# Kernel optimization log

Hardware: AMD Instinct MI355X
Metric: run time of the kernel (lower is better)

## Reference

```python
import jax, jax.numpy as jnp
import numpy as np

DIM = 1024
HEADS = 16
DIM_HEAD = 64
INNER = HEADS * DIM_HEAD
SCALE = DIM_HEAD ** -0.5


def rotate_half(t):
    # '... (j d) -> ... j d' with j=2: split last dim in half
    x1, x2 = jnp.split(t, 2, axis=-1)
    return jnp.concatenate((-x2, x1), axis=-1)


def rotary_pos(n, d, dtype):
    inv_freq = 1.0 / (10000.0 ** (jnp.arange(0, d, 2, dtype=jnp.float32) / d))
    freqs = jnp.arange(n, dtype=jnp.float32)[:, None] * inv_freq[None, :]  # (n, d/2)
    return jnp.concatenate((freqs, freqs), axis=-1).astype(dtype)  # (n, d)


def apply_rope(pos, t):
    return t * jnp.cos(pos) + rotate_half(t) * jnp.sin(pos)


def setup_inputs() -> dict:
    key = jax.random.key(0)
    ks = jax.random.split(key, 5)
    x = jax.random.normal(ks[0], (2, 2048, DIM), dtype=jnp.float32)
    gamma = jnp.ones((DIM,), dtype=jnp.float32)
    beta = jnp.zeros((DIM,), dtype=jnp.float32)
    Wq = jax.random.normal(ks[1], (DIM, INNER), dtype=jnp.float32) * 0.02
    Wkv = jax.random.normal(ks[2], (DIM, 2 * INNER), dtype=jnp.float32) * 0.02
    Wo = jax.random.normal(ks[3], (INNER, DIM), dtype=jnp.float32) * 0.02
    return {"x": x, "gamma": gamma, "beta": beta, "Wq": Wq, "Wkv": Wkv, "Wo": Wo}


def reference(x, gamma, beta, Wq, Wkv, Wo):
    b, n, _ = x.shape
    # LayerNorm with learned gamma, fixed-zero beta buffer
    mu = jnp.mean(x, axis=-1, keepdims=True)
    var = jnp.var(x, axis=-1, keepdims=True)
    xn = (x - mu) / jnp.sqrt(var + 1e-5) * gamma + beta

    q = xn @ Wq                       # (b, n, inner)
    kv = xn @ Wkv
    k, v = jnp.split(kv, 2, axis=-1)

    def to_heads(t):
        return t.reshape(b, n, HEADS, DIM_HEAD).transpose(0, 2, 1, 3)  # b h n d

    q, k, v = map(to_heads, (q, k, v))

    pos = rotary_pos(n, DIM_HEAD, x.dtype)  # (n, d)
    q = apply_rope(pos, q)
    k = apply_rope(pos, k)

    q = q * SCALE
    sim = jnp.einsum('bhid,bhjd->bhij', q, k)

    neg = -jnp.finfo(sim.dtype).max
    causal_mask = jnp.triu(jnp.ones((n, n), dtype=bool), k=1)
    sim = jnp.where(causal_mask, neg, sim)

    attn = jax.nn.softmax(sim, axis=-1)
    out = jnp.einsum('bhij,bhjd->bhid', attn, v)
    out = out.transpose(0, 2, 1, 3).reshape(b, n, INNER)
    return out @ Wo
```

## Files before the change

kernel.cpp:

```cpp
#include <hip/hip_runtime.h>
#include <stdint.h>

typedef unsigned short u16;
typedef __attribute__((ext_vector_type(8))) short short8;
typedef __attribute__((ext_vector_type(4))) float floatx4;
typedef __attribute__((ext_vector_type(4))) unsigned short u16x4;
typedef __attribute__((ext_vector_type(2))) unsigned int uint2v;

__device__ __forceinline__ float bf2f(u16 v) {
  union { uint32_t u; float f; } x; x.u = ((uint32_t)v) << 16; return x.f;
}
__device__ __forceinline__ u16 f2bf(float f) {
  union { float f; uint32_t u; } x; x.f = f;
  uint32_t r = x.u + 0x7fffu + ((x.u >> 16) & 1u);
  return (u16)(r >> 16);
}
__device__ __forceinline__ uint32_t fu(float f) {
  union { float f; uint32_t u; } x; x.f = f; return x.u;
}

#define GL2LDS(g, l)                                                          \
  __builtin_amdgcn_global_load_lds(                                           \
      (const __attribute__((address_space(1))) void*)(g),                     \
      (__attribute__((address_space(3))) void*)(l), 16, 0, 0)

#define WAITBAR(N)                                                            \
  asm volatile("s_waitcnt vmcnt(" #N ")\n\ts_barrier" ::: "memory")
#define BARX asm volatile("s_barrier" ::: "memory")
#define VM0BARX asm volatile("s_waitcnt vmcnt(0)\n\ts_barrier" ::: "memory")

__global__ __launch_bounds__(256) void prep_k(const float* __restrict__ x,
                                              const float* __restrict__ gamma,
                                              const float* __restrict__ beta,
                                              const float* __restrict__ Wq,
                                              const float* __restrict__ Wkv,
                                              const float* __restrict__ Wo,
                                              u16* __restrict__ xn,
                                              u16* __restrict__ wqkvT,
                                              u16* __restrict__ woT) {
  int bid = blockIdx.x;
  int t = threadIdx.x;
  if (bid < 4096) {
    int row = bid;
    const float* xr = x + (size_t)row * 1024;
    float4 xv = *(const float4*)(xr + t * 4);
    float v0 = xv.x, v1 = xv.y, v2 = xv.z, v3 = xv.w;
    float s = v0 + v1 + v2 + v3;
    float s2 = v0 * v0 + v1 * v1 + v2 * v2 + v3 * v3;
#pragma unroll
    for (int d = 1; d < 64; d <<= 1) {
      s += __shfl_xor(s, d, 64);
      s2 += __shfl_xor(s2, d, 64);
    }
    __shared__ float red[8];
    int lane = t & 63, wv = t >> 6;
    if (lane == 0) { red[wv] = s; red[4 + wv] = s2; }
    __syncthreads();
    s = red[0] + red[1] + red[2] + red[3];
    s2 = red[4] + red[5] + red[6] + red[7];
    float mu = s * (1.0f / 1024.0f);
    float var = s2 * (1.0f / 1024.0f) - mu * mu;
    float rstd = rsqrtf(var + 1e-5f);
    float4 gv = *(const float4*)(gamma + t * 4);
    float4 bv = *(const float4*)(beta + t * 4);
    u16x4 ov;
    ov.x = f2bf((v0 - mu) * rstd * gv.x + bv.x);
    ov.y = f2bf((v1 - mu) * rstd * gv.y + bv.y);
    ov.z = f2bf((v2 - mu) * rstd * gv.z + bv.z);
    ov.w = f2bf((v3 - mu) * rstd * gv.w + bv.w);
    *(u16x4*)(xn + (size_t)row * 1024 + t * 4) = ov;
  } else {
    __shared__ float tile[32][33];
    int wb = bid - 4096;
    const float* in;
    u16* outp;
    int C;
    if (wb < 1024) { in = Wq; outp = wqkvT; C = 1024; }
    else if (wb < 3072) { wb -= 1024; in = Wkv; outp = wqkvT + 1024 * 1024; C = 2048; }
    else { wb -= 3072; in = Wo; outp = woT; C = 1024; }
    int nbx = C >> 5;
    int c0 = (wb % nbx) * 32, r0 = (wb / nbx) * 32;
    int tx = t & 31, ty = t >> 5;
#pragma unroll
    for (int i = 0; i < 32; i += 8)
      tile[ty + i][tx] = in[(size_t)(r0 + ty + i) * C + c0 + tx];
    __syncthreads();
#pragma unroll
    for (int i = 0; i < 32; i += 8)
      outp[(size_t)(c0 + ty + i) * 1024 + r0 + tx] = f2bf(tile[tx][ty + i]);
  }
}

__global__ __launch_bounds__(512, 1) void gemm_qkv_k(const u16* __restrict__ A,
                                                     const u16* __restrict__ BT,
                                                     u16* __restrict__ C) {
  __shared__ __align__(16) u16 sA[2][128 * 64];
  __shared__ __align__(16) u16 sB[2][384 * 64];
  int tid = threadIdx.x;
  int w = tid >> 6, l = tid & 63;
  int lr = l & 15, lq = l >> 4;
  int wm = w >> 1, wn = w & 1;
  int bm = blockIdx.y * 128;
  int bn = blockIdx.x * 384;
  floatx4 acc[2][12] = {};
  int gcol = ((tid & 7) ^ ((tid >> 3) & 7)) * 8;
  int strow = tid >> 3;
  int t8 = tid * 8;
  const u16* gA = A + (size_t)(bm + strow) * 1024 + gcol;
  const u16* gB = BT + (size_t)(bn + strow) * 1024 + gcol;
  int csw = (lr & 7) << 3;
  int ar = (wm * 32 + lr) * 64;
  int br = (wn * 192 + lr) * 64;

#define ST_A(bi)                                                              \
  { GL2LDS(gA, &sA[bi][t8]); GL2LDS(gA + 65536, &sA[bi][t8 + 4096]); }
#define ST_B(bi)                                                              \
  { GL2LDS(gB, &sB[bi][t8]);                                                  \
    GL2LDS(gB + 65536, &sB[bi][t8 + 4096]);                                   \
    GL2LDS(gB + 131072, &sB[bi][t8 + 8192]);                                  \
    GL2LDS(gB + 196608, &sB[bi][t8 + 12288]);                                 \
    GL2LDS(gB + 262144, &sB[bi][t8 + 16384]);                                 \
    GL2LDS(gB + 327680, &sB[bi][t8 + 20480]); }
#define HALF(p, kh)                                                           \
  {                                                                           \
    int co_ = ((kh)*32 + lq * 8) ^ csw;                                       \
    short8 a0_ = *(const short8*)&sA[p][ar + co_];                            \
    short8 a1_ = *(const short8*)&sA[p][ar + 1024 + co_];                     \
    _Pragma("unroll") for (int g = 0; g < 3; g++) {                           \
      short8 b0_ = *(const short8*)&sB[p][br + (g * 4 + 0) * 1024 + co_];     \
      short8 b1_ = *(const short8*)&sB[p][br + (g * 4 + 1) * 1024 + co_];     \
      short8 b2_ = *(const short8*)&sB[p][br + (g * 4 + 2) * 1024 + co_];     \
      short8 b3_ = *(const short8*)&sB[p][br + (g * 4 + 3) * 1024 + co_];     \
      acc[0][g*4+0] = __builtin_amdgcn_mfma_f32_16x16x32_bf16(a0_, b0_, acc[0][g*4+0], 0, 0, 0); \
      acc[1][g*4+0] = __builtin_amdgcn_mfma_f32_16x16x32_bf16(a1_, b0_, acc[1][g*4+0], 0, 0, 0); \
      acc[0][g*4+1] = __builtin_amdgcn_mfma_f32_16x16x32_bf16(a0_, b1_, acc[0][g*4+1], 0, 0, 0); \
      acc[1][g*4+1] = __builtin_amdgcn_mfma_f32_16x16x32_bf16(a1_, b1_, acc[1][g*4+1], 0, 0, 0); \
      acc[0][g*4+2] = __builtin_amdgcn_mfma_f32_16x16x32_bf16(a0_, b2_, acc[0][g*4+2], 0, 0, 0); \
      acc[1][g*4+2] = __builtin_amdgcn_mfma_f32_16x16x32_bf16(a1_, b2_, acc[1][g*4+2], 0, 0, 0); \
      acc[0][g*4+3] = __builtin_amdgcn_mfma_f32_16x16x32_bf16(a0_, b3_, acc[0][g*4+3], 0, 0, 0); \
      acc[1][g*4+3] = __builtin_amdgcn_mfma_f32_16x16x32_bf16(a1_, b3_, acc[1][g*4+3], 0, 0, 0); \
    }                                                                         \
  }
#define KT(p, q, DOST)                                                        \
  {                                                                           \
    if (DOST) { ST_A(q); ST_B(q); gA += 64; gB += 64; }                       \
    BARX; __builtin_amdgcn_s_setprio(1);                                      \
    HALF(p, 0);                                                               \
    __builtin_amdgcn_s_setprio(0); BARX;                                      \
    __builtin_amdgcn_s_setprio(1);                                            \
    HALF(p, 1);                                                               \
    __builtin_amdgcn_s_setprio(0); VM0BARX;                                   \
  }

  ST_A(0); ST_B(0); gA += 64; gB += 64;
  VM0BARX;
#pragma unroll 1
  for (int t = 0; t < 7; ++t) {
    KT(0, 1, 1);
    KT(1, 0, 1);
  }
  KT(0, 1, 1);
  KT(1, 0, 0);

#pragma unroll
  for (int nig = 0; nig < 3; nig++) {
    int col0 = bn + wn * 192 + nig * 64;
    int sec = col0 >> 10;
    if (sec == 2) {
#pragma unroll
      for (int p4 = 0; p4 < 4; p4++) {
        int ni = nig * 4 + p4;
        int col = col0 + p4 * 16 + lr;
        int cv = col - 2048;
#pragma unroll
        for (int mi = 0; mi < 2; mi++) {
          int row = bm + wm * 32 + mi * 16 + lq * 4;
          int bq = row >> 11;
          int n = row & 2047;
          int bh = (bq << 4) | (cv >> 6);
          int d = cv & 63;
          size_t L = ((size_t)(bh * 64 + d) << 11) + n;
          u16x4 ov;
          ov.x = f2bf(acc[mi][ni][0]);
          ov.y = f2bf(acc[mi][ni][1]);
          ov.z = f2bf(acc[mi][ni][2]);
          ov.w = f2bf(acc[mi][ni][3]);
          *(u16x4*)(C + (L >> 10) * 3072 + 2048 + (L & 1023)) = ov;
        }
      }
    } else {
      float QS = (sec == 0) ? 0.125f * 1.44269504088896f : 1.0f;
#pragma unroll
      for (int np = 0; np < 2; np++) {
        int i = np * 16 + lr;
        float invf = exp2f(-(float)i * 0.4152410118609203f);
#pragma unroll
        for (int mi = 0; mi < 2; mi++)
#pragma unroll
          for (int r = 0; r < 4; r++) {
            int row = bm + wm * 32 + mi * 16 + lq * 4 + r;
            int n = row & 2047;
            float ang = (float)n * invf;
            float s_, c_;
            __sincosf(ang, &s_, &c_);
            float x1 = acc[mi][nig * 4 + np][r];
            float x2 = acc[mi][nig * 4 + np + 2][r];
            int col = col0 + np * 16 + lr;
            C[(size_t)row * 3072 + col] = f2bf((x1 * c_ - x2 * s_) * QS);
            C[(size_t)row * 3072 + col + 32] = f2bf((x2 * c_ + x1 * s_) * QS);
          }
      }
    }
  }
}

__global__ __launch_bounds__(256) void gemm64_bf16_k(const u16* __restrict__ A,
                                                     const u16* __restrict__ BT,
                                                     float* __restrict__ C,
                                                     int K, int lda, int ldc) {
  __shared__ __align__(16) u16 lA[3][64 * 32];
  __shared__ __align__(16) u16 lB[3][128 * 32];
  int tid = threadIdx.x;
  int bm = blockIdx.y * 64;
  int bn = blockIdx.x * 128;
  int w = tid >> 6, l = tid & 63;
  int wm = (w >> 1) * 32, wn = (w & 1) * 64;
  int lr = l & 15, lq = l >> 4;
  floatx4 acc[2][4] = {};
  int sr = w * 16 + (l >> 2);
  int sc = (l & 3) * 8;
  int sds = sr * 32 + sc;
  const u16* pA0 = A + (size_t)(bm + sr) * lda + sc;
  const u16* pB0 = BT + (size_t)(bn + sr) * K + sc;
  const u16* pB1 = pB0 + (size_t)64 * K;
  int ao[2], bo[4];
#pragma unroll
  for (int i = 0; i < 2; i++) ao[i] = (wm + i * 16 + lr) * 32 + lq * 8;
#pragma unroll
  for (int i = 0; i < 4; i++) bo[i] = (wn + i * 16 + lr) * 32 + lq * 8;

#define STAGE_O(bi)                                                           \
  {                                                                           \
    GL2LDS(pA0, &lA[bi][sds]);                                                \
    GL2LDS(pB0, &lB[bi][sds]);                                                \
    GL2LDS(pB1, &lB[bi][sds + 2048]);                                         \
    pA0 += 32; pB0 += 32; pB1 += 32;                                          \
  }
#define COMPUTE_O(bi)                                                         \
  {                                                                           \
    short8 afr[2], bfr[4];                                                    \
    _Pragma("unroll") for (int i = 0; i < 2; i++)                             \
        afr[i] = *(const short8*)(&lA[bi][ao[i]]);                            \
    _Pragma("unroll") for (int i = 0; i < 4; i++)                             \
        bfr[i] = *(const short8*)(&lB[bi][bo[i]]);                            \
    _Pragma("unroll") for (int mi = 0; mi < 2; mi++)                          \
        _Pragma("unroll") for (int ni = 0; ni < 4; ni++)                      \
            acc[mi][ni] = __builtin_amdgcn_mfma_f32_16x16x32_bf16(            \
                afr[mi], bfr[ni], acc[mi][ni], 0, 0, 0);                      \
  }

  STAGE_O(0);
  STAGE_O(1);
#pragma unroll 1
  for (int t = 0; t < 10; ++t) {
    WAITBAR(3); STAGE_O(2); COMPUTE_O(0);
    WAITBAR(3); STAGE_O(0); COMPUTE_O(1);
    WAITBAR(3); STAGE_O(1); COMPUTE_O(2);
  }
  WAITBAR(3); COMPUTE_O(0);
  WAITBAR(0); COMPUTE_O(1);

#pragma unroll
  for (int mi = 0; mi < 2; mi++)
#pragma unroll
    for (int ni = 0; ni < 4; ni++)
#pragma unroll
      for (int r = 0; r < 4; r++) {
        int row = bm + wm + mi * 16 + lq * 4 + r;
        int col = bn + wn + ni * 16 + lr;
        C[(size_t)row * ldc + col] = acc[mi][ni][r];
      }
}

#define LPT 64
__device__ __forceinline__ void attn_tile2(const u16* lK, const u16* lV, u16* lp,
                                           const short8* aq, floatx4* o,
                                           float& l_i, int lr, int lq,
                                           bool diag, int q0, int k0g,
                                           short8 ones) {
  floatx4 s[4];
#pragma unroll
  for (int ni = 0; ni < 4; ni++) {
    floatx4 a = {};
#pragma unroll
    for (int kc = 0; kc < 2; kc++) {
      int R = ni * 16 + lr;
      int c8 = (kc * 4 + lq) ^ (R & 7);
      short8 kf = *(const short8*)&lK[R * 64 + c8 * 8];
      a = __builtin_amdgcn_mfma_f32_16x16x32_bf16(kf, aq[kc], a, 0, 0, 0);
    }
    s[ni] = a;
  }
  if (diag) {
    int qg = q0 + lr;
#pragma unroll
    for (int ni = 0; ni < 4; ni++)
#pragma unroll
      for (int r = 0; r < 4; r++) {
        int kg = k0g + ni * 16 + lq * 4 + r;
        if (kg > qg) s[ni][r] = -1e30f;
      }
  }
  int swz = (lr & 7) << 3;
#pragma unroll
  for (int ni = 0; ni < 4; ni++) {
    float p0 = exp2f(s[ni][0]), p1 = exp2f(s[ni][1]);
    float p2 = exp2f(s[ni][2]), p3 = exp2f(s[ni][3]);
    uint2v dw;
    dw.x = __builtin_amdgcn_perm(fu(p1), fu(p0), 0x07060302u);
    dw.y = __builtin_amdgcn_perm(fu(p3), fu(p2), 0x07060302u);
    *(uint2v*)&lp[lr * LPT + ((ni * 16 + lq * 4) ^ swz)] = dw;
  }
  short8 pb0 = *(const short8*)&lp[lr * LPT + ((lq * 8) ^ swz)];
  short8 pb1 = *(const short8*)&lp[lr * LPT + ((32 + lq * 8) ^ swz)];
  floatx4 z = {};
  z = __builtin_amdgcn_mfma_f32_16x16x32_bf16(ones, pb0, z, 0, 0, 0);
  z = __builtin_amdgcn_mfma_f32_16x16x32_bf16(ones, pb1, z, 0, 0, 0);
  l_i += z[0];
#pragma unroll
  for (int di = 0; di < 4; di++) {
    int R = di * 16 + lr;
    int c80 = lq ^ (R & 7);
    int c81 = (4 + lq) ^ (R & 7);
    short8 v0 = *(const short8*)&lV[R * 64 + c80 * 8];
    o[di] = __builtin_amdgcn_mfma_f32_16x16x32_bf16(v0, pb0, o[di], 0, 0, 0);
    short8 v1 = *(const short8*)&lV[R * 64 + c81 * 8];
    o[di] = __builtin_amdgcn_mfma_f32_16x16x32_bf16(v1, pb1, o[di], 0, 0, 0);
  }
}

__global__ __launch_bounds__(256) void attn_k(const u16* __restrict__ qkv,
                                              u16* __restrict__ out) {
  __shared__ __align__(16) u16 lK[2][64 * 64];
  __shared__ __align__(16) u16 lV[2][64 * 64];
  __shared__ __align__(16) u16 lP[4][16 * LPT];
  int bh = blockIdx.x;
  int b = bh >> 4, h = bh & 15;
  int y = blockIdx.y;
  int g = y >> 3, o_ = y & 7;
  int j = (g & 1) ? ((g << 3) + 7 - o_) : y;
  int tid = threadIdx.x;
  int w = tid >> 6, l = tid & 63;
  int lr = l & 15, lq = l >> 4;
  int q0 = j * 64 + w * 16;
  const u16* qb = qkv + (size_t)b * 2048 * 3072 + h * 64;
  const u16* kb = qkv + (size_t)b * 2048 * 3072 + 1024 + h * 64;
  int bh64 = bh * 64;
  short8 aq[2];
  aq[0] = *(const short8*)(qb + (size_t)(q0 + lr) * 3072 + lq * 8);
  aq[1] = *(const short8*)(qb + (size_t)(q0 + lr) * 3072 + 32 + lq * 8);
  short8 ones;
#pragma unroll
  for (int i = 0; i < 8; i++) ones[i] = (short)0x3F80;
  floatx4 o[4] = {};
  float l_ = 0.0f;
  int srow8 = l >> 3;
  int sc8 = (l & 7) ^ srow8;
  u16* lp = &lP[w][0];
  int row0 = w * 8 + srow8;
  int row1 = (w + 4) * 8 + srow8;
  const u16* kp0 = kb + (size_t)row0 * 3072 + sc8 * 8;
  const u16* kp1 = kb + (size_t)row1 * 3072 + sc8 * 8;
  const u16* vp0 = qkv + (size_t)((bh64 + row0) * 2) * 3072 + 2048 + sc8 * 8;
  const u16* vp1 = qkv + (size_t)((bh64 + row1) * 2) * 3072 + 2048 + sc8 * 8;
  auto stage = [&](int bufi) {
    GL2LDS(kp0, &lK[bufi][w * 512]);
    GL2LDS(vp0, &lV[bufi][w * 512]);
    GL2LDS(kp1, &lK[bufi][(w + 4) * 512]);
    GL2LDS(vp1, &lV[bufi][(w + 4) * 512]);
  };
  auto advance = [&](int ktStaged) {
    kp0 += 196608; kp1 += 196608;
    int dv = (((ktStaged + 1) & 15) == 0) ? 2112 : 64;
    vp0 += dv; vp1 += dv;
  };
  stage(0);
  advance(0);
  for (int kt = 0; kt <= j; ++kt) {
    int cur = kt & 1;
    __syncthreads();
    if (kt < j) { stage(cur ^ 1); advance(kt + 1); }
    attn_tile2(lK[cur], lV[cur], lp, aq, o, l_, lr, lq, kt == j, q0, kt * 64,
               ones);
  }
  float rl = 1.0f / l_;
#pragma unroll
  for (int di = 0; di < 4; di++) {
    uint2v dw;
    u16 a0 = f2bf(o[di][0] * rl), a1 = f2bf(o[di][1] * rl);
    u16 a2 = f2bf(o[di][2] * rl), a3 = f2bf(o[di][3] * rl);
    dw.x = (uint32_t)a0 | ((uint32_t)a1 << 16);
    dw.y = (uint32_t)a2 | ((uint32_t)a3 << 16);
    int dcol = h * 64 + di * 16 + lq * 4;
    *(uint2v*)(out + ((size_t)(b * 2048 + q0 + lr)) * 1024 + dcol) = dw;
  }
}

extern "C" void kernel_launch(void* const* d_in, const int* in_sizes, int n_in,
                              void* d_out, int out_size, void* d_ws, size_t ws_size,
                              hipStream_t stream) {
  const float* x = (const float*)d_in[0];
  const float* gamma = (const float*)d_in[1];
  const float* beta = (const float*)d_in[2];
  const float* Wq = (const float*)d_in[3];
  const float* Wkv = (const float*)d_in[4];
  const float* Wo = (const float*)d_in[5];
  float* out = (float*)d_out;
  char* ws = (char*)d_ws;

  u16* qkv = (u16*)(ws);
  u16* wqkvT = (u16*)(ws + 25165824);
  u16* woT = (u16*)(ws + 31457280);
  u16* xn = (u16*)(ws + 33554432);
  u16* attn_out = xn;

  prep_k<<<8192, 256, 0, stream>>>(x, gamma, beta, Wq, Wkv, Wo, xn, wqkvT, woT);
  gemm_qkv_k<<<dim3(8, 32), 512, 0, stream>>>(xn, wqkvT, qkv);
  attn_k<<<dim3(32, 32), 256, 0, stream>>>(qkv, attn_out);
  gemm64_bf16_k<<<dim3(8, 64), 256, 0, stream>>>(attn_out, woT, out, 1024, 1024, 1024);
}
```

Measured before the change: 183.3 us.

## Retile output projection GEMM to 128x128 tiles with 512 threads and swizzled LDS

Rewrites the output-projection GEMM to use 128x128 block tiles, 8 waves per block, a K-step of 64 with double buffering, and an XOR-swizzled LDS layout. It also adds s_setprio around the MFMA sections. This mirrors the QKV GEMM structure and aims for more data reuse per block and fewer LDS bank conflicts. In exchange the grid shrinks from 512 to 256 blocks, which may leave some compute units underused. Dimensions are now hardcoded to 1024.

```diff
diff --git a/kernel.cpp b/kernel.cpp
--- a/kernel.cpp
+++ b/kernel.cpp
@@ -214,72 +214,80 @@
   }
 }
 
-__global__ __launch_bounds__(256) void gemm64_bf16_k(const u16* __restrict__ A,
-                                                     const u16* __restrict__ BT,
-                                                     float* __restrict__ C,
-                                                     int K, int lda, int ldc) {
-  __shared__ __align__(16) u16 lA[3][64 * 32];
-  __shared__ __align__(16) u16 lB[3][128 * 32];
+__global__ __launch_bounds__(512, 1) void gemm64_bf16_k(const u16* __restrict__ A,
+                                                        const u16* __restrict__ BT,
+                                                        float* __restrict__ C) {
+  __shared__ __align__(16) u16 sA[2][128 * 64];
+  __shared__ __align__(16) u16 sB[2][128 * 64];
   int tid = threadIdx.x;
-  int bm = blockIdx.y * 64;
+  int w = tid >> 6, l = tid & 63;
+  int lr = l & 15, lq = l >> 4;
+  int wm = w >> 1, wn = w & 1;
+  int bm = blockIdx.y * 128;
   int bn = blockIdx.x * 128;
-  int w = tid >> 6, l = tid & 63;
-  int wm = (w >> 1) * 32, wn = (w & 1) * 64;
-  int lr = l & 15, lq = l >> 4;
   floatx4 acc[2][4] = {};
-  int sr = w * 16 + (l >> 2);
-  int sc = (l & 3) * 8;
-  int sds = sr * 32 + sc;
-  const u16* pA0 = A + (size_t)(bm + sr) * lda + sc;
-  const u16* pB0 = BT + (size_t)(bn + sr) * K + sc;
-  const u16* pB1 = pB0 + (size_t)64 * K;
-  int ao[2], bo[4];
-#pragma unroll
-  for (int i = 0; i < 2; i++) ao[i] = (wm + i * 16 + lr) * 32 + lq * 8;
-#pragma unroll
-  for (int i = 0; i < 4; i++) bo[i] = (wn + i * 16 + lr) * 32 + lq * 8;
-
-#define STAGE_O(bi)                                                           \
+  int gcol = ((tid & 7) ^ ((tid >> 3) & 7)) * 8;
+  int strow = tid >> 3;
+  int t8 = tid * 8;
+  const u16* gA = A + (size_t)(bm + strow) * 1024 + gcol;
+  const u16* gB = BT + (size_t)(bn + strow) * 1024 + gcol;
+  int csw = (lr & 7) << 3;
+  int ar = (wm * 32 + lr) * 64;
+  int br = (wn * 64 + lr) * 64;
+
+#define ST_A2(bi)                                                             \
+  { GL2LDS(gA, &sA[bi][t8]); GL2LDS(gA + 65536, &sA[bi][t8 + 4096]); }
+#define ST_B2(bi)                                                             \
+  { GL2LDS(gB, &sB[bi][t8]); GL2LDS(gB + 65536, &sB[bi][t8 + 4096]); }
+#define HALF2(p, kh)                                                          \
   {                                                                           \
-    GL2LDS(pA0, &lA[bi][sds]);                                                \
-    GL2LDS(pB0, &lB[bi][sds]);                                                \
-    GL2LDS(pB1, &lB[bi][sds + 2048]);                                         \
-    pA0 += 32; pB0 += 32; pB1 += 32;                                          \
-  }
-#define COMPUTE_O(bi)                                                         \
+    int co_ = ((kh)*32 + lq * 8) ^ csw;                                       \
+    short8 a0_ = *(const short8*)&sA[p][ar + co_];                            \
+    short8 a1_ = *(const short8*)&sA[p][ar + 1024 + co_];                     \
+    short8 b0_ = *(const short8*)&sB[p][br + 0 + co_];                        \
+    short8 b1_ = *(const short8*)&sB[p][br + 1024 + co_];                     \
+    short8 b2_ = *(const short8*)&sB[p][br + 2048 + co_];                     \
+    short8 b3_ = *(const short8*)&sB[p][br + 3072 + co_];                     \
+    acc[0][0] = __builtin_amdgcn_mfma_f32_16x16x32_bf16(a0_, b0_, acc[0][0], 0, 0, 0); \
+    acc[1][0] = __builtin_amdgcn_mfma_f32_16x16x32_bf16(a1_, b0_, acc[1][0], 0, 0, 0); \
+    acc[0][1] = __builtin_amdgcn_mfma_f32_16x16x32_bf16(a0_, b1_, acc[0][1], 0, 0, 0); \
+    acc[1][1] = __builtin_amdgcn_mfma_f32_16x16x32_bf16(a1_, b1_, acc[1][1], 0, 0, 0); \
+    acc[0][2] = __builtin_amdgcn_mfma_f32_16x16x32_bf16(a0_, b2_, acc[0][2], 0, 0, 0); \
+    acc[1][2] = __builtin_amdgcn_mfma_f32_16x16x32_bf16(a1_, b2_, acc[1][2], 0, 0, 0); \
+    acc[0][3] = __builtin_amdgcn_mfma_f32_16x16x32_bf16(a0_, b3_, acc[0][3], 0, 0, 0); \
+    acc[1][3] = __builtin_amdgcn_mfma_f32_16x16x32_bf16(a1_, b3_, acc[1][3], 0, 0, 0); \
+  }
+#define KT2(p, q, DOST)                                                       \
   {                                                                           \
-    short8 afr[2], bfr[4];                                                    \
-    _Pragma("unroll") for (int i = 0; i < 2; i++)                             \
-        afr[i] = *(const short8*)(&lA[bi][ao[i]]);                            \
-    _Pragma("unroll") for (int i = 0; i < 4; i++)                             \
-        bfr[i] = *(const short8*)(&lB[bi][bo[i]]);                            \
-    _Pragma("unroll") for (int mi = 0; mi < 2; mi++)                          \
-        _Pragma("unroll") for (int ni = 0; ni < 4; ni++)                      \
-            acc[mi][ni] = __builtin_amdgcn_mfma_f32_16x16x32_bf16(            \
-                afr[mi], bfr[ni], acc[mi][ni], 0, 0, 0);                      \
-  }
-
-  STAGE_O(0);
-  STAGE_O(1);
+    if (DOST) { ST_A2(q); ST_B2(q); gA += 64; gB += 64; }                     \
+    BARX; __builtin_amdgcn_s_setprio(1);                                      \
+    HALF2(p, 0);                                                              \
+    __builtin_amdgcn_s_setprio(0); BARX;                                      \
+    __builtin_amdgcn_s_setprio(1);                                            \
+    HALF2(p, 1);                                                              \
+    __builtin_amdgcn_s_setprio(0); VM0BARX;                                   \
+  }
+
+  ST_A2(0); ST_B2(0); gA += 64; gB += 64;
+  VM0BARX;
 #pragma unroll 1
-  for (int t = 0; t < 10; ++t) {
-    WAITBAR(3); STAGE_O(2); COMPUTE_O(0);
-    WAITBAR(3); STAGE_O(0); COMPUTE_O(1);
-    WAITBAR(3); STAGE_O(1); COMPUTE_O(2);
-  }
-  WAITBAR(3); COMPUTE_O(0);
-  WAITBAR(0); COMPUTE_O(1);
+  for (int t = 0; t < 7; ++t) {
+    KT2(0, 1, 1);
+    KT2(1, 0, 1);
+  }
+  KT2(0, 1, 1);
+  KT2(1, 0, 0);
 
 #pragma unroll
   for (int mi = 0; mi < 2; mi++)
 #pragma unroll
-    for (int ni = 0; ni < 4; ni++)
-#pragma unroll
-      for (int r = 0; r < 4; r++) {
-        int row = bm + wm + mi * 16 + lq * 4 + r;
-        int col = bn + wn + ni * 16 + lr;
-        C[(size_t)row * ldc + col] = acc[mi][ni][r];
-      }
+    for (int ni = 0; ni < 4; ni++) {
+      int row = bm + wm * 32 + mi * 16 + lq * 4;
+      int col = bn + wn * 64 + ni * 16 + lr;
+#pragma unroll
+      for (int r = 0; r < 4; r++)
+        C[(size_t)(row + r) * 1024 + col] = acc[mi][ni][r];
+    }
 }
 
 #define LPT 64
@@ -427,5 +435,5 @@
   prep_k<<<8192, 256, 0, stream>>>(x, gamma, beta, Wq, Wkv, Wo, xn, wqkvT, woT);
   gemm_qkv_k<<<dim3(8, 32), 512, 0, stream>>>(xn, wqkvT, qkv);
   attn_k<<<dim3(32, 32), 256, 0, stream>>>(qkv, attn_out);
-  gemm64_bf16_k<<<dim3(8, 64), 256, 0, stream>>>(attn_out, woT, out, 1024, 1024, 1024);
-}
+  gemm64_bf16_k<<<dim3(8, 32), 512, 0, stream>>>(attn_out, woT, out);
+}
```

After: 181.4 us. About the same (-1.0%).
